# Kernel optimization log

Hardware: AMD Instinct MI355X
Metric: run time of the kernel (lower is better)

The kernel has to match this reference:

```python
import jax, jax.numpy as jnp
import numpy as np

C = 256   # embedding_dim
B = 16
N = 2048
BN_EPS = 1e-5


def _sa_params(key, c):
    ks = jax.random.split(key, 8)
    s = 1.0 / np.sqrt(c)
    return dict(
        Wq=jax.random.normal(ks[0], (c // 2, c), jnp.float32) * s,
        Wk=jax.random.normal(ks[1], (c // 2, c), jnp.float32) * s,
        Wv=jax.random.normal(ks[2], (c, c), jnp.float32) * s,
        bv=jax.random.normal(ks[3], (c,), jnp.float32) * 0.01,
        Wt=jax.random.normal(ks[4], (c, c), jnp.float32) * s,
        bt=jax.random.normal(ks[5], (c,), jnp.float32) * 0.01,
        gamma=jnp.ones((c,), jnp.float32),
        beta=jnp.zeros((c,), jnp.float32),
    )


def setup_inputs() -> dict:
    key = jax.random.key(0)
    kx, k1, k2 = jax.random.split(key, 3)
    inp = {"x": jax.random.normal(kx, (B, C, N), jnp.float32)}
    for tag, kk in (("1", k1), ("2", k2)):
        for name, v in _sa_params(kk, C).items():
            inp[name + tag] = v
    return inp


def _sa_layer(x, Wq, Wk, Wv, bv, Wt, bt, gamma, beta):
    # 1x1 conv == per-point linear: [B,C,N]
    x_q = jnp.einsum('oc,bcn->bno', Wq, x)            # [B,N,C/2]
    x_k = jnp.einsum('oc,bcn->bon', Wk, x)            # [B,C/2,N]
    x_v = jnp.einsum('oc,bcn->bon', Wv, x) + bv[None, :, None]
    energy = jnp.einsum('bnc,bcm->bnm', x_q, x_k)     # [B,N,N]
    attn = jax.nn.softmax(energy, axis=-1)
    # offset-attention column-wise L1 renorm
    attn = attn / (1e-9 + attn.sum(axis=1, keepdims=True))
    x_r = jnp.einsum('bcn,bnm->bcm', x_v, attn)       # [B,C,N]
    h = x - x_r
    h = jnp.einsum('oc,bcn->bon', Wt, h) + bt[None, :, None]
    # BatchNorm1d (training mode, biased var over batch+points per channel)
    mean = h.mean(axis=(0, 2), keepdims=True)
    var = jnp.mean((h - mean) ** 2, axis=(0, 2), keepdims=True)
    h = (h - mean) * jax.lax.rsqrt(var + BN_EPS)
    h = h * gamma[None, :, None] + beta[None, :, None]
    return x + jax.nn.relu(h)


def reference(x,
              Wq1, Wk1, Wv1, bv1, Wt1, bt1, gamma1, beta1,
              Wq2, Wk2, Wv2, bv2, Wt2, bt2, gamma2, beta2):
    x1 = _sa_layer(x, Wq1, Wk1, Wv1, bv1, Wt1, bt1, gamma1, beta1)
    x2 = _sa_layer(x1, Wq2, Wk2, Wv2, bv2, Wt2, bt2, gamma2, beta2)
    return jnp.concatenate((x1, x2), axis=1)          # [B,2C,N]
```

## Files before the change

kernel.cpp:

```cpp
#include <hip/hip_runtime.h>

#define DI __device__ __forceinline__

typedef _Float16 f16_t;
typedef _Float16 f16x8 __attribute__((ext_vector_type(8)));
typedef float    f32x4 __attribute__((ext_vector_type(4)));

static_assert(sizeof(f16x8) == 16, "f16x8 must be 16B");

#define B_  16
#define C_  256
#define CH_ 128
#define N_  2048

DI f32x4 fzero(){ f32x4 z = {0.f,0.f,0.f,0.f}; return z; }
DI f16x8 ldg8(const f16_t* p){ return *(const f16x8*)p; }
DI f32x4 mfma16(f16x8 a, f16x8 b, f32x4 c){
  return __builtin_amdgcn_mfma_f32_16x16x32_f16(a, b, c, 0, 0, 0);
}
DI void split2(float v, f16_t& hi, f16_t& lo){
  hi = (f16_t)v; lo = (f16_t)(v - (float)hi);
}
DI int swz_b(int i){ return ((i&7)<<1) | ((i>>3)&1); }

#define GLL16(src, dst) __builtin_amdgcn_global_load_lds( \
    (const __attribute__((address_space(1))) void*)(src), \
    (__attribute__((address_space(3))) void*)(dst), 16, 0, 0)

__global__ void k_wconv(const float* q1,const float* k1,const float* v1,const float* t1,
                        const float* q2,const float* k2,const float* v2,const float* t2,
                        f16_t* out){
  int i = blockIdx.x*256 + threadIdx.x;
  int l = (i >= 196608) ? 1 : 0;
  int r = i - l*196608;
  const float* s; long dbase;
  if(r < 32768){ s = l? q2:q1; dbase = 0; }
  else if(r < 65536){ r -= 32768; s = l? k2:k1; dbase = 65536; }
  else if(r < 131072){ r -= 65536; s = l? v2:v1; dbase = 131072; }
  else { r -= 131072; s = l? t2:t1; dbase = 262144; }
  int o = r >> 8, c = r & 255;
  float v = s[o*256 + c];
  f16_t hi, lo; split2(v, hi, lo);
  f16_t* d = out + (long)l*393216 + dbase + (long)o*512;
  d[c] = hi; d[c+256] = lo;
}

__global__ void k_transpose(const float* __restrict__ X, long bstride,
                            f16_t* __restrict__ XtS){
  int b = blockIdx.x, n0 = blockIdx.y*32, c0 = blockIdx.z*64;
  __shared__ float tl[32][65];
  int t = threadIdx.x;
  int nn = t & 31, cr = t >> 5;
  const float* src = X + (long)b*bstride + n0 + nn;
  #pragma unroll
  for(int i=0;i<8;i++){
    int cc = cr + i*8;
    tl[nn][cc] = src[(long)(c0+cc)*N_];
  }
  __syncthreads();
  int n2 = t >> 3, cq = (t & 7)*8;
  __align__(16) f16_t hi8[8], lo8[8];
  #pragma unroll
  for(int j=0;j<8;j++) split2(tl[n2][cq+j], hi8[j], lo8[j]);
  f16_t* dst = XtS + ((long)b*N_ + n0 + n2)*512 + c0 + cq;
  *(f16x8*)dst         = *(f16x8*)hi8;
  *(f16x8*)(dst + 256) = *(f16x8*)lo8;
}

template<int LGX, int SPLIT_OUT, int BIAS, int DUAL>
__global__ __launch_bounds__(256) void k_gemm3(
    const f16_t* __restrict__ A, long sA,
    const f16_t* __restrict__ Bt, long sB,
    f16_t* __restrict__ out, int ldo, long sO,
    const float* __restrict__ bias, long dualoff)
{
  int i = blockIdx.x;
  int b = swz_b(i);
  int r = i>>4;
  int m0 = (r & ((1<<LGX)-1))*64, n0 = (r >> LGX)*64;
  int t = threadIdx.x, w = t>>6, l = t&63, lr = l&15, lg = l>>4;
  const f16_t* Ab = A + (long)b*sA + (long)(m0 + w*16 + lr)*512;
  const f16_t* Bb = Bt + (long)b*sB;
  f32x4 acc[4];
  #pragma unroll
  for(int i2=0;i2<4;i2++) acc[i2] = fzero();
  for(int k=0;k<256;k+=32){
    f16x8 ah = ldg8(Ab + k + lg*8);
    f16x8 al = ldg8(Ab + 256 + k + lg*8);
    #pragma unroll
    for(int ns=0;ns<4;ns++){
      const f16_t* brow = Bb + (long)(n0 + ns*16 + lr)*512;
      f16x8 bh = ldg8(brow + k + lg*8);
      f16x8 bl = ldg8(brow + 256 + k + lg*8);
      acc[ns] = mfma16(ah, bh, acc[ns]);
      acc[ns] = mfma16(ah, bl, acc[ns]);
      acc[ns] = mfma16(al, bh, acc[ns]);
    }
  }
  f16_t* ob = out + (long)b*sO;
  #pragma unroll
  for(int ns=0;ns<4;ns++){
    #pragma unroll
    for(int j=0;j<4;j++){
      int row = m0 + w*16 + lg*4 + j;
      int col = n0 + ns*16 + lr;
      float v = acc[ns][j];
      if(BIAS) v += bias[row];
      if(SPLIT_OUT){
        f16_t hi, lo; split2(v, hi, lo);
        f16_t* base = ob;
        if(DUAL && col >= 128) base = ob + (dualoff - 128);
        base[(long)row*ldo + col]       = hi;
        base[(long)row*ldo + col + 128] = lo;
      } else {
        ob[(long)row*ldo + col] = (f16_t)v;
      }
    }
  }
}

__global__ __launch_bounds__(512) void k_rowstats(
    const f16_t* __restrict__ xqS, const f16_t* __restrict__ xkS,
    float* __restrict__ rowoff)
{
  extern __shared__ __align__(16) char smem[];
  const int bi = blockIdx.x;
  const int b = swz_b(bi);
  const int n0 = (bi>>4)*128;
  const int t = threadIdx.x, w = t>>6, l = t&63, lr = l&15, lg = l>>4;

  const f16_t* qp = xqS + ((long)b*N_ + n0 + w*16 + lr)*256;
  f16x8 bqh[4], bql[4];
  #pragma unroll
  for(int k=0;k<4;k++){
    bqh[k] = ldg8(qp + k*32 + lg*8);
    bql[k] = ldg8(qp + 128 + k*32 + lg*8);
  }
  const f16_t* kb = xkS + (long)b*N_*256;

  const int krow_off = l>>5, kslot = l&31;
  const f16_t *ks0, *ks1;
  { int row0 = w*2 + krow_off;
    ks0 = kb + (long)row0*256 + ((kslot ^ (row0&15))*8);
    int row1 = 16 + w*2 + krow_off;
    ks1 = kb + (long)row1*256 + ((kslot ^ (row1&15))*8); }

  #define KSTAGE(buf) do { char* kd = smem + (buf)*16384;                     \
    GLL16(ks0, kd + w*1024); GLL16(ks1, kd + 8192 + w*1024); } while(0)

  float rmax = -3e38f, rsum = 0.f;
  KSTAGE(0);

  #pragma unroll 1
  for(int i=0; i<64; i++){
    const int cur = i&1, nxt = cur^1;
    if(i<63){
      ks0 += 8192; ks1 += 8192;
      KSTAGE(nxt);
      asm volatile("s_waitcnt vmcnt(2)" ::: "memory");
    } else {
      asm volatile("s_waitcnt vmcnt(0)" ::: "memory");
    }
    asm volatile("s_barrier" ::: "memory");
    const char* kbuf = smem + cur*16384;
    #pragma unroll
    for(int s=0;s<2;s++){
      const char* krow = kbuf + (s*16 + lr)*512;
      f16x8 ah[4], al_[4];
      #pragma unroll
      for(int k=0;k<4;k++){
        ah[k]  = *(const f16x8*)(krow + ((((4*k+lg) ^ lr))<<4));
        al_[k] = *(const f16x8*)(krow + ((16 + (((4*k+lg)) ^ lr))<<4));
      }
      f32x4 a1 = fzero(), a2 = fzero(), a3 = fzero();
      #pragma unroll
      for(int k=0;k<4;k++) a1 = mfma16(ah[k],  bqh[k], a1);
      #pragma unroll
      for(int k=0;k<4;k++) a2 = mfma16(ah[k],  bql[k], a2);
      #pragma unroll
      for(int k=0;k<4;k++) a3 = mfma16(al_[k], bqh[k], a3);
      f32x4 acc = (a1 + a2) + a3;
      float vm = fmaxf(fmaxf(acc[0],acc[1]), fmaxf(acc[2],acc[3]));
      float nm = fmaxf(rmax, vm);
      rsum = rsum*__expf(rmax-nm)
           + __expf(acc[0]-nm)+__expf(acc[1]-nm)+__expf(acc[2]-nm)+__expf(acc[3]-nm);
      rmax = nm;
    }
    asm volatile("s_barrier" ::: "memory");
  }
  #undef KSTAGE

  #pragma unroll
  for(int off=16; off<64; off<<=1){
    float om = __shfl_xor(rmax, off, 64);
    float os = __shfl_xor(rsum, off, 64);
    float nm = fmaxf(rmax, om);
    rsum = rsum*__expf(rmax-nm) + os*__expf(om-nm);
    rmax = nm;
  }
  if(lg==0) rowoff[(long)b*N_ + n0 + w*16 + lr] = rmax + __logf(rsum);
}

__global__ __launch_bounds__(256) void k_apply(
    const f16_t* __restrict__ xqS, const f16_t* __restrict__ xkS,
    const f16_t* __restrict__ xv, const float* __restrict__ rowoff,
    const float* __restrict__ X, long xbstride, f16_t* __restrict__ h0T)
{
  extern __shared__ __align__(16) char smem[];
  const int bi = blockIdx.x;
  const int b = swz_b(bi);
  const int m0 = (bi>>4)*64;
  const int t = threadIdx.x, w = t>>6, l = t&63, lr = l&15, lg = l>>4;
  float* ro_s = (float*)(smem + 65536);
  {
    const float* rob = rowoff + (long)b*N_;
    *(f32x4*)(ro_s + t*4)        = *(const f32x4*)(rob + t*4);
    *(f32x4*)(ro_s + t*4 + 1024) = *(const f32x4*)(rob + t*4 + 1024);
  }

  const f16_t* akp = xkS + ((long)b*N_ + m0 + w*16 + lr)*256;
  f16x8 akh[4], akl[4];
  #pragma unroll
  for(int k=0;k<4;k++){
    akh[k] = ldg8(akp + k*32 + lg*8);
    akl[k] = ldg8(akp + 128 + k*32 + lg*8);
  }

  const f16_t* xqb = xqS + (long)b*N_*256;
  const f16_t* xvb = xv + (long)b*C_*N_;
  const int qperm = ((lr>>2)*8 + (lr&3));

  const int qrow_off = (l>>5), qslot = l&31;
  const int vc_off = (l>>2), vslot = l&3;

  #define STAGE(nn, nxtbuf) do {                                              \
    char* qd = smem + (nxtbuf)*16384;                                         \
    char* vd = smem + 32768 + (nxtbuf)*16384;                                 \
    _Pragma("unroll")                                                         \
    for(int r=0;r<4;r++){                                                     \
      int qrow = (r*4+w)*2 + qrow_off;                                        \
      int qsw  = (qrow&3) | (((qrow>>3)&3)<<2);                               \
      const f16_t* qsrc = xqb + (long)((nn) + qrow)*256 + ((qslot ^ qsw)*8);  \
      GLL16(qsrc, qd + (r*4+w)*1024);                                         \
      int vc = (r*4+w)*16 + vc_off;                                           \
      const f16_t* vsrc2 = xvb + (long)vc*N_ + (nn) + ((vslot ^ (vc&3))*8);   \
      GLL16(vsrc2, vd + (r*4+w)*1024);                                        \
    }                                                                         \
  } while(0)

  f32x4 y[16];
  #pragma unroll
  for(int i2=0;i2<16;i2++) y[i2] = fzero();
  float cs = 0.f, cm = -3e38f;

  __syncthreads();
  STAGE(0, 0);

  const int vsl = (lg ^ (lr&3)) << 4;

  #pragma unroll 1
  for(int i=0; i<64; i++){
    const int cur = i&1, nxt = cur^1;
    const int n0 = i*32;
    const int nn = (i<63) ? (n0+32) : 0;
    STAGE(nn, nxt);
    asm volatile("s_waitcnt vmcnt(8)" ::: "memory");
    asm volatile("s_barrier" ::: "memory");
    const char* qb = smem + cur*16384;
    const char* vb = smem + 32768 + cur*16384;
    float g[2][4];
    #pragma unroll
    for(int s2=0;s2<2;s2++){
      const int rl = qperm + s2*4;
      const char* qrow = qb + rl*512;
      f16x8 qh[4], ql[4];
      #pragma unroll
      for(int k=0;k<4;k++){
        qh[k] = *(const f16x8*)(qrow + (((4*k + lg) ^ lr)<<4));
        ql[k] = *(const f16x8*)(qrow + 256 + (((4*k + lg) ^ lr)<<4));
      }
      f32x4 e1 = fzero(), e2 = fzero(), e3 = fzero();
      #pragma unroll
      for(int k=0;k<4;k++) e1 = mfma16(qh[k], akh[k], e1);
      #pragma unroll
      for(int k=0;k<4;k++) e2 = mfma16(ql[k], akh[k], e2);
      #pragma unroll
      for(int k=0;k<4;k++) e3 = mfma16(qh[k], akl[k], e3);
      f32x4 e = (e1 + e2) + e3;
      f32x4 ro4 = *(const f32x4*)(ro_s + n0 + lg*8 + s2*4);
      #pragma unroll
      for(int j=0;j<4;j++) g[s2][j] = e[j] - ro4[j];
    }
    float v = fmaxf(fmaxf(fmaxf(g[0][0],g[0][1]), fmaxf(g[0][2],g[0][3])),
                    fmaxf(fmaxf(g[1][0],g[1][1]), fmaxf(g[1][2],g[1][3])));
    v = fmaxf(v, __shfl_xor(v, 16, 64));
    v = fmaxf(v, __shfl_xor(v, 32, 64));
    bool need = v > cm + 8.f;
    float fj = need ? __expf(cm - v) : 1.f;
    if(need) cm = v;
    cs *= fj;
    __align__(16) f16_t pv[8];
    #pragma unroll
    for(int s2=0;s2<2;s2++){
      #pragma unroll
      for(int j=0;j<4;j++){
        float p = __expf(g[s2][j] - cm);
        f16_t pb = (f16_t)p;
        cs += (float)pb;
        pv[s2*4+j] = pb;
      }
    }
    f16x8 pfrag = *(const f16x8*)pv;
    if(__any(need)){
      #pragma unroll
      for(int cf=0;cf<16;cf++){
        #pragma unroll
        for(int j2=0;j2<4;j2++) y[cf][j2] *= fj;
      }
    }
    #pragma unroll
    for(int cf=0;cf<16;cf++){
      f16x8 av = *(const f16x8*)(vb + (cf*16 + lr)*64 + vsl);
      y[cf] = mfma16(av, pfrag, y[cf]);
    }
    asm volatile("s_barrier" ::: "memory");
  }
  #undef STAGE

  cs += __shfl_xor(cs, 16, 64);
  cs += __shfl_xor(cs, 32, 64);
  float inv = 1.f/(1e-9f*__expf(-cm) + cs);

  f16_t* H = (f16_t*)(smem + 49152);
  const int mq = t&63, cq = t>>6;
  const float* Xb = X + (long)b*xbstride + m0;
  uint4* dstb = (uint4*)(h0T + ((long)b*N_ + m0)*C_);
  #pragma unroll
  for(int half=0; half<2; half++){
    #pragma unroll
    for(int cf8=0; cf8<8; cf8++){
      int cf = half*8 + cf8;
      #pragma unroll
      for(int j=0;j<4;j++){
        int cl = cf8*16 + lg*4 + j;
        int m  = w*16 + lr;
        *(f16_t*)((char*)H + m*256 + ((((cl>>3) ^ (m&7))<<4) | ((cl&7)<<1)))
          = (f16_t)(y[cf][j]*inv);
      }
    }
    __syncthreads();
    #pragma unroll 4
    for(int ci=0; ci<32; ci++){
      int cl = cq*32 + ci;
      int c  = half*128 + cl;
      f16_t* hp = (f16_t*)((char*)H + mq*256 + ((((cl>>3) ^ (mq&7))<<4) | ((cl&7)<<1)));
      *hp = (f16_t)(Xb[(long)c*N_ + mq] - (float)*hp);
    }
    __syncthreads();
    {
      const uint4* src = (const uint4*)H;
      for(int i2=t;i2<1024;i2+=256){
        int row = i2>>4, slot = i2&15;
        dstb[row*32 + half*16 + slot] = src[(i2 & ~15) | (slot ^ (row&7))];
      }
    }
    __syncthreads();
  }
}

__global__ __launch_bounds__(256) void k_wt_bn(
    const f16_t* __restrict__ WtS, const f16_t* __restrict__ h0T,
    const float* __restrict__ bt,
    f16_t* __restrict__ h1, float* __restrict__ bnacc)
{
  int i = blockIdx.x;
  int b = swz_b(i);
  int r = i>>4;
  int o0 = (r&3)*64, m0 = (r>>2)*64;
  int t=threadIdx.x, w=t>>6, l=t&63, lr=l&15, lg=l>>4;
  const f16_t* Arow = WtS + (long)(o0 + w*16 + lr)*512;
  const f16_t* Bb = h0T + (long)b*N_*C_;
  f32x4 acc[4];
  #pragma unroll
  for(int i2=0;i2<4;i2++) acc[i2] = fzero();
  for(int k=0;k<C_;k+=32){
    f16x8 afh = ldg8(Arow + k + lg*8);
    f16x8 afl = ldg8(Arow + 256 + k + lg*8);
    #pragma unroll
    for(int ms=0;ms<4;ms++){
      f16x8 bf_ = ldg8(Bb + (long)(m0 + ms*16 + lr)*C_ + k + lg*8);
      acc[ms] = mfma16(afh, bf_, acc[ms]);
      acc[ms] = mfma16(afl, bf_, acc[ms]);
    }
  }
  float s1[4]={0.f,0.f,0.f,0.f}, s2v[4]={0.f,0.f,0.f,0.f};
  f16_t* h1b = h1 + (long)b*C_*N_;
  #pragma unroll
  for(int j=0;j<4;j++){
    int o = o0 + w*16 + lg*4 + j;
    float bias = bt[o];
    #pragma unroll
    for(int ms=0;ms<4;ms++){
      float v = acc[ms][j] + bias;
      h1b[(long)o*N_ + m0 + ms*16 + lr] = (f16_t)v;
      s1[j] += v; s2v[j] += v*v;
    }
  }
  #pragma unroll
  for(int off=1; off<16; off<<=1){
    #pragma unroll
    for(int j=0;j<4;j++){ s1[j]+=__shfl_xor(s1[j],off,64); s2v[j]+=__shfl_xor(s2v[j],off,64); }
  }
  if(lr==0){
    #pragma unroll
    for(int j=0;j<4;j++){
      int o = o0 + w*16 + lg*4 + j;
      atomicAdd(&bnacc[o], s1[j]);
      atomicAdd(&bnacc[256+o], s2v[j]);
    }
  }
}

__global__ void k_out(const f16_t* __restrict__ h1, const float* __restrict__ X, long xbstride,
                      const float* __restrict__ bnacc, const float* __restrict__ gamma,
                      const float* __restrict__ beta, float* __restrict__ out, long ocoff){
  long i = (long)blockIdx.x*256 + threadIdx.x;
  long e = i*8;
  int b = (int)(e >> 19);
  int rem = (int)(e & 524287);
  int c = rem >> 11;
  float mean = bnacc[c] * (1.f/32768.f);
  float var  = bnacc[256+c] * (1.f/32768.f) - mean*mean;
  float sc = gamma[c] * rsqrtf(var + 1e-5f);
  float sh = beta[c] - mean*sc;
  f16x8 hv = *(const f16x8*)(h1 + e);
  const float* xb = X + (long)b*xbstride + rem;
  float4 xr0 = *(const float4*)xb;
  float4 xr1 = *(const float4*)(xb + 4);
  float4 o0, o1;
  o0.x = xr0.x + fmaxf(fmaf((float)hv[0], sc, sh), 0.f);
  o0.y = xr0.y + fmaxf(fmaf((float)hv[1], sc, sh), 0.f);
  o0.z = xr0.z + fmaxf(fmaf((float)hv[2], sc, sh), 0.f);
  o0.w = xr0.w + fmaxf(fmaf((float)hv[3], sc, sh), 0.f);
  o1.x = xr1.x + fmaxf(fmaf((float)hv[4], sc, sh), 0.f);
  o1.y = xr1.y + fmaxf(fmaf((float)hv[5], sc, sh), 0.f);
  o1.z = xr1.z + fmaxf(fmaf((float)hv[6], sc, sh), 0.f);
  o1.w = xr1.w + fmaxf(fmaf((float)hv[7], sc, sh), 0.f);
  float* ob = out + (long)b*(512L*N_) + ocoff + rem;
  *(float4*)ob       = o0;
  *(float4*)(ob + 4) = o1;
}

extern "C" void kernel_launch(void* const* d_in, const int* in_sizes, int n_in,
                              void* d_out, int out_size, void* d_ws, size_t ws_size,
                              hipStream_t stream){
  (void)in_sizes; (void)n_in; (void)out_size; (void)ws_size;
  const float* x = (const float*)d_in[0];
  const float *Wf[2][4], *bv[2], *bt[2], *gm[2], *bb[2];
  for(int l=0;l<2;l++){
    int base = 1 + l*8;
    Wf[l][0]=(const float*)d_in[base+0];
    Wf[l][1]=(const float*)d_in[base+1];
    Wf[l][2]=(const float*)d_in[base+2];
    bv[l]   =(const float*)d_in[base+3];
    Wf[l][3]=(const float*)d_in[base+4];
    bt[l]   =(const float*)d_in[base+5];
    gm[l]   =(const float*)d_in[base+6];
    bb[l]   =(const float*)d_in[base+7];
  }
  char* ws = (char*)d_ws;
  size_t off = 0;
  auto alloc = [&](size_t bytes){ size_t o = off; off += (bytes + 255) & ~(size_t)255; return o; };
  size_t oXt = alloc((size_t)B_*N_*512*2);
  size_t oXq = alloc((size_t)B_*N_*256*2);
  size_t oXk = alloc((size_t)B_*N_*256*2);
  size_t oXv = alloc((size_t)B_*C_*N_*2);
  size_t oH0 = alloc((size_t)B_*N_*C_*2);
  size_t oRo = alloc((size_t)B_*N_*4);
  size_t oBn = alloc(2*512*4);
  size_t oW  = alloc((size_t)786432*2);

  hipMemsetAsync(ws + oBn, 0, 2*512*4, stream);
  k_wconv<<<1536,256,0,stream>>>(Wf[0][0],Wf[0][1],Wf[0][2],Wf[0][3],
                                 Wf[1][0],Wf[1][1],Wf[1][2],Wf[1][3],
                                 (f16_t*)(ws+oW));
  float* dout = (float*)d_out;
  f16_t* H1 = (f16_t*)(ws + oXq);
  const long XKOFF = ((long)(oXk - oXq)) / 2;
  for(int l=0;l<2;l++){
    const float* Xl = l ? dout : x;
    long xbs = l ? 512L*N_ : 256L*N_;
    const f16_t* WqS = (const f16_t*)(ws+oW) + (size_t)l*393216;
    const f16_t* WvS = WqS + 131072;
    const f16_t* WtS = WqS + 262144;
    f16_t* XtS = (f16_t*)(ws+oXt);
    f16_t* Xq  = (f16_t*)(ws+oXq);
    f16_t* Xk  = (f16_t*)(ws+oXk);
    f16_t* Xv  = (f16_t*)(ws+oXv);
    f16_t* H0  = (f16_t*)(ws+oH0);
    float* Ro  = (float*)(ws+oRo);
    float* Bn  = (float*)(ws+oBn) + l*512;

    k_transpose<<<dim3(B_, N_/32, C_/64),256,0,stream>>>(Xl, xbs, XtS);
    k_gemm3<5,1,0,1><<<2048,256,0,stream>>>(XtS, (long)N_*512, WqS, 0L,
                                            Xq, 256, (long)N_*256, nullptr, XKOFF);
    k_gemm3<2,0,1,0><<<2048,256,0,stream>>>(WvS, 0L, XtS, (long)N_*512,
                                            Xv, N_, (long)C_*N_, bv[l], 0L);
    k_rowstats<<<256,512,32768,stream>>>(Xq, Xk, Ro);
    k_apply<<<512,256,73728,stream>>>(Xq, Xk, Xv, Ro, Xl, xbs, H0);
    k_wt_bn<<<2048,256,0,stream>>>(WtS, H0, bt[l], H1, Bn);
    k_out<<<4096,256,0,stream>>>(H1, Xl, xbs, Bn, gm[l], bb[l], dout, (long)l*C_*N_);
  }
}
```

Baseline: 858.4 us.

## Load Q fragments directly into registers, stage only V through LDS

In the attention-apply kernel, Q rows are now read from global memory straight into double-buffered register arrays instead of being staged through shared memory. Only the V tile still goes through LDS, and the loop is unrolled by two so the register buffers can alternate. The aim is to cut LDS footprint (73728 down to 40960 bytes) and LDS read traffic, which can allow higher occupancy. In exchange, each wave issues redundant global loads of Q and holds 32 extra f16x8 registers, so register pressure rises and occupancy may fall.

```diff
diff --git a/kernel.cpp b/kernel.cpp
--- a/kernel.cpp
+++ b/kernel.cpp
@@ -211,7 +211,7 @@
   const int b = swz_b(bi);
   const int m0 = (bi>>4)*64;
   const int t = threadIdx.x, w = t>>6, l = t&63, lr = l&15, lg = l>>4;
-  float* ro_s = (float*)(smem + 65536);
+  float* ro_s = (float*)(smem + 32768);
   {
     const float* rob = rowoff + (long)b*N_;
     *(f32x4*)(ro_s + t*4)        = *(const f32x4*)(rob + t*4);
@@ -229,109 +229,125 @@
   const f16_t* xqb = xqS + (long)b*N_*256;
   const f16_t* xvb = xv + (long)b*C_*N_;
   const int qperm = ((lr>>2)*8 + (lr&3));
-
-  const int qrow_off = (l>>5), qslot = l&31;
   const int vc_off = (l>>2), vslot = l&3;
 
-  #define STAGE(nn, nxtbuf) do {                                              \
-    char* qd = smem + (nxtbuf)*16384;                                         \
-    char* vd = smem + 32768 + (nxtbuf)*16384;                                 \
+  #define STAGEV(nn, buf) do {                                                \
+    char* vd = smem + (buf)*16384;                                            \
     _Pragma("unroll")                                                         \
     for(int r=0;r<4;r++){                                                     \
-      int qrow = (r*4+w)*2 + qrow_off;                                        \
-      int qsw  = (qrow&3) | (((qrow>>3)&3)<<2);                               \
-      const f16_t* qsrc = xqb + (long)((nn) + qrow)*256 + ((qslot ^ qsw)*8);  \
-      GLL16(qsrc, qd + (r*4+w)*1024);                                         \
       int vc = (r*4+w)*16 + vc_off;                                           \
       const f16_t* vsrc2 = xvb + (long)vc*N_ + (nn) + ((vslot ^ (vc&3))*8);   \
       GLL16(vsrc2, vd + (r*4+w)*1024);                                        \
     }                                                                         \
   } while(0)
 
+  #define QLOAD(dst, nn) do {                                                 \
+    _Pragma("unroll")                                                         \
+    for(int s2=0;s2<2;s2++){                                                  \
+      const f16_t* qr = xqb + (long)((nn) + qperm + s2*4)*256 + lg*8;         \
+      _Pragma("unroll")                                                       \
+      for(int k=0;k<4;k++){                                                   \
+        dst[s2*8+k]   = ldg8(qr + k*32);                                      \
+        dst[s2*8+4+k] = ldg8(qr + 128 + k*32);                                \
+      }                                                                       \
+    }                                                                         \
+  } while(0)
+
   f32x4 y[16];
   #pragma unroll
   for(int i2=0;i2<16;i2++) y[i2] = fzero();
   float cs = 0.f, cm = -3e38f;
 
+  #define CHUNK(n0c, qreg, vbuf) do {                                         \
+    const char* vb = smem + (vbuf)*16384;                                     \
+    float g[2][4];                                                            \
+    _Pragma("unroll")                                                         \
+    for(int s2=0;s2<2;s2++){                                                  \
+      f32x4 e1 = fzero(), e2 = fzero(), e3 = fzero();                         \
+      _Pragma("unroll")                                                       \
+      for(int k=0;k<4;k++) e1 = mfma16(qreg[s2*8+k],   akh[k], e1);           \
+      _Pragma("unroll")                                                       \
+      for(int k=0;k<4;k++) e2 = mfma16(qreg[s2*8+4+k], akh[k], e2);           \
+      _Pragma("unroll")                                                       \
+      for(int k=0;k<4;k++) e3 = mfma16(qreg[s2*8+k],   akl[k], e3);           \
+      f32x4 e = (e1 + e2) + e3;                                               \
+      f32x4 ro4 = *(const f32x4*)(ro_s + (n0c) + lg*8 + s2*4);                \
+      _Pragma("unroll")                                                       \
+      for(int j=0;j<4;j++) g[s2][j] = e[j] - ro4[j];                          \
+    }                                                                         \
+    float v = fmaxf(fmaxf(fmaxf(g[0][0],g[0][1]), fmaxf(g[0][2],g[0][3])),    \
+                    fmaxf(fmaxf(g[1][0],g[1][1]), fmaxf(g[1][2],g[1][3])));   \
+    v = fmaxf(v, __shfl_xor(v, 16, 64));                                      \
+    v = fmaxf(v, __shfl_xor(v, 32, 64));                                      \
+    bool need = v > cm + 8.f;                                                 \
+    float fj = need ? __expf(cm - v) : 1.f;                                   \
+    if(need) cm = v;                                                          \
+    cs *= fj;                                                                 \
+    __align__(16) f16_t pv[8];                                                \
+    _Pragma("unroll")                                                         \
+    for(int s2=0;s2<2;s2++){                                                  \
+      _Pragma("unroll")                                                       \
+      for(int j=0;j<4;j++){                                                   \
+        float p = __expf(g[s2][j] - cm);                                      \
+        f16_t pb = (f16_t)p;                                                  \
+        cs += (float)pb;                                                      \
+        pv[s2*4+j] = pb;                                                      \
+      }                                                                       \
+    }                                                                         \
+    f16x8 pfrag = *(const f16x8*)pv;                                          \
+    if(__any(need)){                                                          \
+      _Pragma("unroll")                                                       \
+      for(int cf=0;cf<16;cf++){                                               \
+        _Pragma("unroll")                                                     \
+        for(int j2=0;j2<4;j2++) y[cf][j2] *= fj;                              \
+      }                                                                       \
+    }                                                                         \
+    _Pragma("unroll")                                                         \
+    for(int cf=0;cf<16;cf++){                                                 \
+      f16x8 av = *(const f16x8*)(vb + (cf*16 + lr)*64 + vsl);                 \
+      y[cf] = mfma16(av, pfrag, y[cf]);                                       \
+    }                                                                         \
+  } while(0)
+
+  const int vsl = (lg ^ (lr&3)) << 4;
+
+  f16x8 qA[16], qB[16];
   __syncthreads();
-  STAGE(0, 0);
-
-  const int vsl = (lg ^ (lr&3)) << 4;
+  QLOAD(qA, 0);
+  STAGEV(0, 0);
 
   #pragma unroll 1
-  for(int i=0; i<64; i++){
-    const int cur = i&1, nxt = cur^1;
-    const int n0 = i*32;
-    const int nn = (i<63) ? (n0+32) : 0;
-    STAGE(nn, nxt);
-    asm volatile("s_waitcnt vmcnt(8)" ::: "memory");
-    asm volatile("s_barrier" ::: "memory");
-    const char* qb = smem + cur*16384;
-    const char* vb = smem + 32768 + cur*16384;
-    float g[2][4];
-    #pragma unroll
-    for(int s2=0;s2<2;s2++){
-      const int rl = qperm + s2*4;
-      const char* qrow = qb + rl*512;
-      f16x8 qh[4], ql[4];
-      #pragma unroll
-      for(int k=0;k<4;k++){
-        qh[k] = *(const f16x8*)(qrow + (((4*k + lg) ^ lr)<<4));
-        ql[k] = *(const f16x8*)(qrow + 256 + (((4*k + lg) ^ lr)<<4));
+  for(int i=0; i<64; i+=2){
+    {
+      QLOAD(qB, (i+1)*32);
+      STAGEV((i+1)*32, 1);
+      asm volatile("s_waitcnt vmcnt(20)" ::: "memory");
+      asm volatile("s_barrier" ::: "memory");
+      CHUNK(i*32, qA, 0);
+      asm volatile("s_barrier" ::: "memory");
+    }
+    {
+      if(i+2 < 64){
+        QLOAD(qA, (i+2)*32);
+        STAGEV((i+2)*32, 0);
+        asm volatile("s_waitcnt vmcnt(20)" ::: "memory");
+      } else {
+        asm volatile("s_waitcnt vmcnt(0)" ::: "memory");
       }
-      f32x4 e1 = fzero(), e2 = fzero(), e3 = fzero();
-      #pragma unroll
-      for(int k=0;k<4;k++) e1 = mfma16(qh[k], akh[k], e1);
-      #pragma unroll
-      for(int k=0;k<4;k++) e2 = mfma16(ql[k], akh[k], e2);
-      #pragma unroll
-      for(int k=0;k<4;k++) e3 = mfma16(qh[k], akl[k], e3);
-      f32x4 e = (e1 + e2) + e3;
-      f32x4 ro4 = *(const f32x4*)(ro_s + n0 + lg*8 + s2*4);
-      #pragma unroll
-      for(int j=0;j<4;j++) g[s2][j] = e[j] - ro4[j];
-    }
-    float v = fmaxf(fmaxf(fmaxf(g[0][0],g[0][1]), fmaxf(g[0][2],g[0][3])),
-                    fmaxf(fmaxf(g[1][0],g[1][1]), fmaxf(g[1][2],g[1][3])));
-    v = fmaxf(v, __shfl_xor(v, 16, 64));
-    v = fmaxf(v, __shfl_xor(v, 32, 64));
-    bool need = v > cm + 8.f;
-    float fj = need ? __expf(cm - v) : 1.f;
-    if(need) cm = v;
-    cs *= fj;
-    __align__(16) f16_t pv[8];
-    #pragma unroll
-    for(int s2=0;s2<2;s2++){
-      #pragma unroll
-      for(int j=0;j<4;j++){
-        float p = __expf(g[s2][j] - cm);
-        f16_t pb = (f16_t)p;
-        cs += (float)pb;
-        pv[s2*4+j] = pb;
-      }
-    }
-    f16x8 pfrag = *(const f16x8*)pv;
-    if(__any(need)){
-      #pragma unroll
-      for(int cf=0;cf<16;cf++){
-        #pragma unroll
-        for(int j2=0;j2<4;j2++) y[cf][j2] *= fj;
-      }
-    }
-    #pragma unroll
-    for(int cf=0;cf<16;cf++){
-      f16x8 av = *(const f16x8*)(vb + (cf*16 + lr)*64 + vsl);
-      y[cf] = mfma16(av, pfrag, y[cf]);
-    }
-    asm volatile("s_barrier" ::: "memory");
-  }
-  #undef STAGE
+      asm volatile("s_barrier" ::: "memory");
+      CHUNK((i+1)*32, qB, 1);
+      asm volatile("s_barrier" ::: "memory");
+    }
+  }
+  #undef CHUNK
+  #undef QLOAD
+  #undef STAGEV
 
   cs += __shfl_xor(cs, 16, 64);
   cs += __shfl_xor(cs, 32, 64);
   float inv = 1.f/(1e-9f*__expf(-cm) + cs);
 
-  f16_t* H = (f16_t*)(smem + 49152);
+  f16_t* H = (f16_t*)(smem + 16384);
   const int mq = t&63, cq = t>>6;
   const float* Xb = X + (long)b*xbstride + m0;
   uint4* dstb = (uint4*)(h0T + ((long)b*N_ + m0)*C_);
@@ -507,7 +523,7 @@
     k_gemm3<2,0,1,0><<<2048,256,0,stream>>>(WvS, 0L, XtS, (long)N_*512,
                                             Xv, N_, (long)C_*N_, bv[l], 0L);
     k_rowstats<<<256,512,32768,stream>>>(Xq, Xk, Ro);
-    k_apply<<<512,256,73728,stream>>>(Xq, Xk, Xv, Ro, Xl, xbs, H0);
+    k_apply<<<512,256,40960,stream>>>(Xq, Xk, Xv, Ro, Xl, xbs, H0);
     k_wt_bn<<<2048,256,0,stream>>>(WtS, H0, bt[l], H1, Bn);
     k_out<<<4096,256,0,stream>>>(H1, Xl, xbs, Bn, gm[l], bb[l], dout, (long)l*C_*N_);
   }
```

Result: slower. 1.308 ms (+52.3%).
